# Kernel optimization log

Hardware: AMD Instinct MI355X
Metric: run time of the kernel (lower is better)

## Reference

```python
import jax, jax.numpy as jnp
import numpy as np

IN_FEATURES = 2048
OUT_FEATURES = 8192


def setup_inputs() -> dict:
    key = jax.random.key(0)
    k_x, k_w, k_s, k_b = jax.random.split(key, 4)
    x = jax.random.normal(k_x, (4, 2048, IN_FEATURES), dtype=jnp.float32)
    # int8 weights as produced by quantize(): values in [-128, 127]
    weight_int8 = jax.random.randint(k_w, (OUT_FEATURES, IN_FEATURES), -128, 128, dtype=jnp.int8)
    # per-output-row scale, shape [out_features, 1]
    scale = jax.random.uniform(k_s, (OUT_FEATURES, 1), dtype=jnp.float32, minval=1e-4, maxval=0.02)
    bias = jax.random.normal(k_b, (OUT_FEATURES,), dtype=jnp.float32) * 0.01
    return {"x": x, "weight_int8": weight_int8, "scale": scale, "bias": bias}


def reference(x, weight_int8, scale, bias):
    # dequantize: [out, in] int8 -> x.dtype, scaled per output row
    weight = weight_int8.astype(x.dtype) * scale.astype(x.dtype)
    # F.linear: x @ weight.T + bias
    return jnp.einsum('bsi,oi->bso', x, weight) + bias.astype(x.dtype)
```

## Files before the change

### kernel.cpp

```cpp
#include <hip/hip_runtime.h>
#include <hip/hip_bf16.h>

#define M_DIM 8192
#define N_DIM 8192
#define K_DIM 2048

#define BK 64
#define NT (K_DIM / BK)
#define SLOT_BYTES 24576

typedef float f32x4 __attribute__((ext_vector_type(4)));
typedef int   i32x4 __attribute__((ext_vector_type(4)));
typedef unsigned int u32;
typedef u32 u32x2 __attribute__((ext_vector_type(2)));
typedef u32 u32x4 __attribute__((ext_vector_type(4)));


__device__ __forceinline__ void gload16(const unsigned char* g, char* l) {
    __builtin_amdgcn_global_load_lds(
        (const __attribute__((address_space(1))) u32*)g,
        (__attribute__((address_space(3))) u32*)l, 16, 0, 0);
}

__device__ __forceinline__ u32 pack4(int a, int b, int c, int d) {
    return (u32)(a & 255) | ((u32)(b & 255) << 8) |
           ((u32)(c & 255) << 16) | ((u32)(d & 255) << 24);
}


__global__ void __launch_bounds__(256) quant_x_k(const float* __restrict__ x,
                                                 unsigned char* __restrict__ xq,
                                                 float* __restrict__ sx) {
    const int row = blockIdx.x;
    const int t = threadIdx.x;
    const float* xr = x + (size_t)row * K_DIM;
    f32x4 v0 = *((const f32x4*)xr + t * 2);
    f32x4 v1 = *((const f32x4*)xr + t * 2 + 1);
    float m = fabsf(v0[0]);
    m = fmaxf(m, fabsf(v0[1])); m = fmaxf(m, fabsf(v0[2])); m = fmaxf(m, fabsf(v0[3]));
    m = fmaxf(m, fabsf(v1[0])); m = fmaxf(m, fabsf(v1[1]));
    m = fmaxf(m, fabsf(v1[2])); m = fmaxf(m, fabsf(v1[3]));
#pragma unroll
    for (int off = 32; off >= 1; off >>= 1)
        m = fmaxf(m, __shfl_xor(m, off, 64));
    __shared__ float wmax[4];
    if ((t & 63) == 0) wmax[t >> 6] = m;
    __syncthreads();
    m = fmaxf(fmaxf(wmax[0], wmax[1]), fmaxf(wmax[2], wmax[3]));
    m = fmaxf(m, 1e-20f);
    const float rs = 127.0f / m;
    const int q0 = (int)rintf(v0[0] * rs), q1 = (int)rintf(v0[1] * rs);
    const int q2 = (int)rintf(v0[2] * rs), q3 = (int)rintf(v0[3] * rs);
    const int q4 = (int)rintf(v1[0] * rs), q5 = (int)rintf(v1[1] * rs);
    const int q6 = (int)rintf(v1[2] * rs), q7 = (int)rintf(v1[3] * rs);
    u32x2 o;
    o[0] = pack4(q0, q1, q2, q3);
    o[1] = pack4(q4, q5, q6, q7);
    *((u32x2*)(xq + (size_t)row * K_DIM) + t) = o;
    if (t == 0) sx[row] = m / 127.0f;
}


__global__ void __launch_bounds__(256) cvt_w_k(const int* __restrict__ w,
                                               unsigned char* __restrict__ wq, int n16) {
    const int stride = gridDim.x * blockDim.x;
    for (int i = blockIdx.x * blockDim.x + threadIdx.x; i < n16; i += stride) {
        const i32x4* p = (const i32x4*)w + (size_t)i * 4;
        i32x4 a = p[0], b = p[1], c = p[2], d = p[3];
        u32x4 o;
        o[0] = pack4(a[0], a[1], a[2], a[3]);
        o[1] = pack4(b[0], b[1], b[2], b[3]);
        o[2] = pack4(c[0], c[1], c[2], c[3]);
        o[3] = pack4(d[0], d[1], d[2], d[3]);
        *((u32x4*)wq + i) = o;
    }
}


__global__ void __launch_bounds__(512, 4)
gemm_i8(const unsigned char* __restrict__ Aq, const unsigned char* __restrict__ Bq,
        const float* __restrict__ sx, const float* __restrict__ sw,
        const float* __restrict__ bias, float* __restrict__ C) {
    extern __shared__ __align__(16) char ldsb[];

    const int bid = blockIdx.x;
    const int swz = (bid & 7) * 256 + (bid >> 3);
    const int rowBase = (swz >> 5) * 128;
    const int colBase = (swz & 31) * 256;

    const int t = threadIdx.x;
    const int l = t & 63;
    const int w = t >> 6;
    const int wm = w >> 2;
    const int wn = w & 3;
    const int fr = l & 15;
    const int s4 = l >> 4;

    const int sr = t >> 2;
    const int sk = (((t & 3) ^ ((sr >> 1) & 3)) * 16);
    const unsigned char* gA0 = Aq + (size_t)(rowBase + sr) * K_DIM + sk;
    const unsigned char* gB0 = Bq + (size_t)(colBase + sr) * K_DIM + sk;
    const unsigned char* gB1 = Bq + (size_t)(colBase + 128 + sr) * K_DIM + sk;

#define STAGE(tk) do { \
        char* _b = ldsb + ((tk) & 1) * SLOT_BYTES; \
        const int _k = (tk) * BK; \
        gload16(gA0 + _k, _b + t * 16); \
        gload16(gB0 + _k, _b + 8192 + t * 16); \
        gload16(gB1 + _k, _b + 16384 + t * 16); \
    } while (0)

    const int pc = ((s4 ^ ((fr >> 1) & 3)) * 16);
    int aoff[4], boff[4];
#pragma unroll
    for (int mi = 0; mi < 4; ++mi)
        aoff[mi] = (wm * 64 + mi * 16 + fr) * 64 + pc;
#pragma unroll
    for (int ni = 0; ni < 4; ++ni)
        boff[ni] = 8192 + (wn * 64 + ni * 16 + fr) * 64 + pc;

    i32x4 acc[4][4] = {};
    i32x4 af[4], bf[4];

#define SB    __builtin_amdgcn_sched_barrier(0)
#define BAR   __builtin_amdgcn_s_barrier()
#define P1    __builtin_amdgcn_s_setprio(1)
#define P0    __builtin_amdgcn_s_setprio(0)
#define LGKM0 asm volatile("s_waitcnt lgkmcnt(0)" ::: "memory")
#define VM3   asm volatile("s_waitcnt vmcnt(3)" ::: "memory")
#define VM0   asm volatile("s_waitcnt vmcnt(0)" ::: "memory")

#define READS(tk) do { \
        const char* _s = ldsb + ((tk) & 1) * SLOT_BYTES; \
        _Pragma("unroll") \
        for (int mi = 0; mi < 4; ++mi) af[mi] = *(const i32x4*)(_s + aoff[mi]); \
        _Pragma("unroll") \
        for (int ni = 0; ni < 4; ++ni) bf[ni] = *(const i32x4*)(_s + boff[ni]); \
    } while (0)

#define MFMA16 do { P1; \
        _Pragma("unroll") \
        for (int mi = 0; mi < 4; ++mi) \
            _Pragma("unroll") \
            for (int ni = 0; ni < 4; ++ni) \
                acc[mi][ni] = __builtin_amdgcn_mfma_i32_16x16x64_i8( \
                    af[mi], bf[ni], acc[mi][ni], 0, 0, 0); \
        P0; } while (0)

    STAGE(0); STAGE(1);
    VM3; SB; BAR; SB;

#pragma unroll
    for (int tk = 0; tk < NT - 2; ++tk) {
        READS(tk);
        LGKM0; SB; BAR; SB;
        STAGE(tk + 2);
        MFMA16;
        VM3; SB; BAR; SB;
    }
    READS(NT - 2);
    LGKM0; SB; BAR; SB;
    MFMA16;
    VM0; SB; BAR; SB;
    READS(NT - 1);
    LGKM0; SB;
    MFMA16;

#undef MFMA16
#undef READS
#undef STAGE

#pragma unroll
    for (int ni = 0; ni < 4; ++ni) {
        const int col = colBase + wn * 64 + ni * 16 + fr;
        const float swc = sw[col];
        const float bz = bias[col];
#pragma unroll
        for (int mi = 0; mi < 4; ++mi) {
            const int rb = rowBase + wm * 64 + mi * 16 + s4 * 4;
            i32x4 a = acc[mi][ni];
#pragma unroll
            for (int r = 0; r < 4; ++r)
                C[(size_t)(rb + r) * N_DIM + col] =
                    (float)a[r] * (sx[rb + r] * swc) + bz;
        }
    }
}


typedef int i32x4_t __attribute__((ext_vector_type(4)));
__global__ void __launch_bounds__(256) naive_k(const float* __restrict__ x,
                                               const int* __restrict__ w,
                                               const float* __restrict__ scale,
                                               const float* __restrict__ bias,
                                               float* __restrict__ out) {
    __shared__ float xs[K_DIM];
    const int m = blockIdx.x >> 5;
    const int n = ((blockIdx.x & 31) << 8) + threadIdx.x;
    for (int i = threadIdx.x; i < K_DIM; i += 256) xs[i] = x[(size_t)m * K_DIM + i];
    __syncthreads();
    const int* wr = w + (size_t)n * K_DIM;
    float acc = 0.f;
    for (int k = 0; k < K_DIM; k += 4) {
        i32x4_t v = *(const i32x4_t*)(wr + k);
        acc += xs[k]     * (float)v[0];
        acc += xs[k + 1] * (float)v[1];
        acc += xs[k + 2] * (float)v[2];
        acc += xs[k + 3] * (float)v[3];
    }
    out[(size_t)m * N_DIM + n] = acc * scale[n] + bias[n];
}


extern "C" void kernel_launch(void* const* d_in, const int* in_sizes, int n_in,
                              void* d_out, int out_size, void* d_ws, size_t ws_size,
                              hipStream_t stream) {
    const float* x     = (const float*)d_in[0];
    const int*   w8    = (const int*)d_in[1];
    const float* sw    = (const float*)d_in[2];
    const float* bias  = (const float*)d_in[3];
    float*       out   = (float*)d_out;

    const size_t xq_bytes = (size_t)M_DIM * K_DIM;
    const size_t wq_bytes = (size_t)N_DIM * K_DIM;
    const size_t need = xq_bytes + wq_bytes + (size_t)M_DIM * sizeof(float);
    if (ws_size >= need) {
        unsigned char* xq = (unsigned char*)d_ws;
        unsigned char* wq = xq + xq_bytes;
        float* sx = (float*)(wq + wq_bytes);
        hipFuncSetAttribute((const void*)gemm_i8,
                            hipFuncAttributeMaxDynamicSharedMemorySize, 2 * SLOT_BYTES);
        quant_x_k<<<M_DIM, 256, 0, stream>>>(x, xq, sx);
        cvt_w_k<<<2048, 256, 0, stream>>>(w8, wq, N_DIM * K_DIM / 16);
        gemm_i8<<<dim3((M_DIM / 128) * (N_DIM / 256)), 512, 2 * SLOT_BYTES, stream>>>(
            xq, wq, sx, sw, bias, out);
    } else {
        naive_k<<<(M_DIM * (N_DIM / 256)), 256, 0, stream>>>(x, w8, sw, bias, out);
    }
}
```

Measured before the change: 245.1 us.

## Use 4 waves per block with 128x64 warp tiles in int8 GEMM

The int8 GEMM block drops from 8 waves to 4, and each wave now computes a 128x64 output tile (8x4 MFMA fragments) instead of 64x64. Each thread issues six 16-byte global-to-LDS loads per stage instead of three, and the K loop is no longer unrolled. The aim is more MFMA work per LDS read of B fragments and fewer waves syncing at each barrier. In exchange, accumulator register pressure doubles and fewer waves are available to hide latency.

```diff
diff --git a/kernel.cpp b/kernel.cpp
--- a/kernel.cpp
+++ b/kernel.cpp
@@ -77,7 +77,7 @@
 }
 
 
-__global__ void __launch_bounds__(512, 4)
+__global__ void __launch_bounds__(256, 2)
 gemm_i8(const unsigned char* __restrict__ Aq, const unsigned char* __restrict__ Bq,
         const float* __restrict__ sx, const float* __restrict__ sw,
         const float* __restrict__ bias, float* __restrict__ C) {
@@ -90,83 +90,87 @@
 
     const int t = threadIdx.x;
     const int l = t & 63;
-    const int w = t >> 6;
-    const int wm = w >> 2;
-    const int wn = w & 3;
+    const int wn = t >> 6;
     const int fr = l & 15;
     const int s4 = l >> 4;
 
     const int sr = t >> 2;
     const int sk = (((t & 3) ^ ((sr >> 1) & 3)) * 16);
     const unsigned char* gA0 = Aq + (size_t)(rowBase + sr) * K_DIM + sk;
+    const unsigned char* gA1 = Aq + (size_t)(rowBase + 64 + sr) * K_DIM + sk;
     const unsigned char* gB0 = Bq + (size_t)(colBase + sr) * K_DIM + sk;
-    const unsigned char* gB1 = Bq + (size_t)(colBase + 128 + sr) * K_DIM + sk;
+    const unsigned char* gB1 = Bq + (size_t)(colBase + 64 + sr) * K_DIM + sk;
+    const unsigned char* gB2 = Bq + (size_t)(colBase + 128 + sr) * K_DIM + sk;
+    const unsigned char* gB3 = Bq + (size_t)(colBase + 192 + sr) * K_DIM + sk;
 
 #define STAGE(tk) do { \
         char* _b = ldsb + ((tk) & 1) * SLOT_BYTES; \
         const int _k = (tk) * BK; \
         gload16(gA0 + _k, _b + t * 16); \
+        gload16(gA1 + _k, _b + 4096 + t * 16); \
         gload16(gB0 + _k, _b + 8192 + t * 16); \
-        gload16(gB1 + _k, _b + 16384 + t * 16); \
+        gload16(gB1 + _k, _b + 12288 + t * 16); \
+        gload16(gB2 + _k, _b + 16384 + t * 16); \
+        gload16(gB3 + _k, _b + 20480 + t * 16); \
     } while (0)
 
     const int pc = ((s4 ^ ((fr >> 1) & 3)) * 16);
-    int aoff[4], boff[4];
-#pragma unroll
-    for (int mi = 0; mi < 4; ++mi)
-        aoff[mi] = (wm * 64 + mi * 16 + fr) * 64 + pc;
+    int aoff[8], boff[4];
+#pragma unroll
+    for (int mi = 0; mi < 8; ++mi)
+        aoff[mi] = (mi * 16 + fr) * 64 + pc;
 #pragma unroll
     for (int ni = 0; ni < 4; ++ni)
         boff[ni] = 8192 + (wn * 64 + ni * 16 + fr) * 64 + pc;
 
-    i32x4 acc[4][4] = {};
-    i32x4 af[4], bf[4];
+    i32x4 acc[8][4] = {};
+    i32x4 af[8], bf[4];
 
 #define SB    __builtin_amdgcn_sched_barrier(0)
 #define BAR   __builtin_amdgcn_s_barrier()
 #define P1    __builtin_amdgcn_s_setprio(1)
-#define P0    __builtin_amdgcn_s_setprio(0)
+#define P0p   __builtin_amdgcn_s_setprio(0)
 #define LGKM0 asm volatile("s_waitcnt lgkmcnt(0)" ::: "memory")
-#define VM3   asm volatile("s_waitcnt vmcnt(3)" ::: "memory")
+#define VM6   asm volatile("s_waitcnt vmcnt(6)" ::: "memory")
 #define VM0   asm volatile("s_waitcnt vmcnt(0)" ::: "memory")
 
 #define READS(tk) do { \
         const char* _s = ldsb + ((tk) & 1) * SLOT_BYTES; \
         _Pragma("unroll") \
-        for (int mi = 0; mi < 4; ++mi) af[mi] = *(const i32x4*)(_s + aoff[mi]); \
+        for (int mi = 0; mi < 8; ++mi) af[mi] = *(const i32x4*)(_s + aoff[mi]); \
         _Pragma("unroll") \
         for (int ni = 0; ni < 4; ++ni) bf[ni] = *(const i32x4*)(_s + boff[ni]); \
     } while (0)
 
-#define MFMA16 do { P1; \
+#define MFMA32 do { P1; \
         _Pragma("unroll") \
-        for (int mi = 0; mi < 4; ++mi) \
+        for (int mi = 0; mi < 8; ++mi) \
             _Pragma("unroll") \
             for (int ni = 0; ni < 4; ++ni) \
                 acc[mi][ni] = __builtin_amdgcn_mfma_i32_16x16x64_i8( \
                     af[mi], bf[ni], acc[mi][ni], 0, 0, 0); \
-        P0; } while (0)
+        P0p; } while (0)
 
     STAGE(0); STAGE(1);
-    VM3; SB; BAR; SB;
-
-#pragma unroll
-    for (int tk = 0; tk < NT - 2; ++tk) {
-        READS(tk);
+    VM6; SB; BAR; SB;
+
+#pragma unroll 1
+    for (int T = 0; T < NT - 2; ++T) {
+        READS(T);
         LGKM0; SB; BAR; SB;
-        STAGE(tk + 2);
-        MFMA16;
-        VM3; SB; BAR; SB;
+        STAGE(T + 2);
+        MFMA32;
+        VM6; SB; BAR; SB;
     }
     READS(NT - 2);
     LGKM0; SB; BAR; SB;
-    MFMA16;
+    MFMA32;
     VM0; SB; BAR; SB;
     READS(NT - 1);
     LGKM0; SB;
-    MFMA16;
-
-#undef MFMA16
+    MFMA32;
+
+#undef MFMA32
 #undef READS
 #undef STAGE
 
@@ -176,8 +180,8 @@
         const float swc = sw[col];
         const float bz = bias[col];
 #pragma unroll
-        for (int mi = 0; mi < 4; ++mi) {
-            const int rb = rowBase + wm * 64 + mi * 16 + s4 * 4;
+        for (int mi = 0; mi < 8; ++mi) {
+            const int rb = rowBase + mi * 16 + s4 * 4;
             i32x4 a = acc[mi][ni];
 #pragma unroll
             for (int r = 0; r < 4; ++r)
@@ -232,7 +236,7 @@
                             hipFuncAttributeMaxDynamicSharedMemorySize, 2 * SLOT_BYTES);
         quant_x_k<<<M_DIM, 256, 0, stream>>>(x, xq, sx);
         cvt_w_k<<<2048, 256, 0, stream>>>(w8, wq, N_DIM * K_DIM / 16);
-        gemm_i8<<<dim3((M_DIM / 128) * (N_DIM / 256)), 512, 2 * SLOT_BYTES, stream>>>(
+        gemm_i8<<<dim3((M_DIM / 128) * (N_DIM / 256)), 256, 2 * SLOT_BYTES, stream>>>(
             xq, wq, sx, sw, bias, out);
     } else {
         naive_k<<<(M_DIM * (N_DIM / 256)), 256, 0, stream>>>(x, w8, sw, bias, out);
```

Result: no change. 249.4 us (+1.8%).
